# Kernel optimization log

Measured on AMD Instinct MI355X. Metric: run time of the kernel, lower is better.

Reference implementation:

```python
import jax, jax.numpy as jnp
import numpy as np

N_NODES = 50000
N_EDGES = 600000
N_FEAT = 128
HIDDEN = 128
OUT_CH = 128
N_GRAPHS = 64
BN_EPS = 1e-5


def gcn_conv(x, src, dst, ew, W, b):
    """PyG GCNConv: add self-loops, symmetric deg^{-1/2} normalization with edge weights."""
    n = x.shape[0]
    h = x @ W  # [N, out]
    loop = jnp.arange(n)
    src2 = jnp.concatenate([src, loop])
    dst2 = jnp.concatenate([dst, loop])
    w2 = jnp.concatenate([ew, jnp.ones((n,), x.dtype)])
    deg = jax.ops.segment_sum(w2, dst2, num_segments=n)
    dinv = jnp.where(deg > 0, jax.lax.rsqrt(deg), 0.0)
    norm = dinv[src2] * w2 * dinv[dst2]  # [E+N]
    out = jax.ops.segment_sum(h[src2] * norm[:, None], dst2, num_segments=n)
    return out + b


def setup_inputs() -> dict:
    key = jax.random.key(0)
    ks = jax.random.split(key, 12)
    x = jax.random.normal(ks[0], (N_NODES, N_FEAT), jnp.float32)
    edge_index = jax.random.randint(ks[1], (2, N_EDGES), 0, N_NODES, dtype=jnp.int64)
    batch = jnp.sort(jax.random.randint(ks[2], (N_NODES,), 0, N_GRAPHS, dtype=jnp.int64))
    edge_attr = jax.random.uniform(ks[3], (N_EDGES,), jnp.float32)
    s1 = 1.0 / np.sqrt(N_FEAT)
    s2 = 1.0 / np.sqrt(HIDDEN)
    s3 = 1.0 / np.sqrt(OUT_CH)
    s4 = 1.0 / np.sqrt(OUT_CH // 2)
    return {
        "x": x, "edge_index": edge_index, "batch": batch, "edge_attr": edge_attr,
        "W1": jax.random.uniform(ks[4], (N_FEAT, HIDDEN), jnp.float32, -s1, s1),
        "b1": jnp.zeros((HIDDEN,), jnp.float32),
        "W2": jax.random.uniform(ks[5], (HIDDEN, OUT_CH), jnp.float32, -s2, s2),
        "b2": jnp.zeros((OUT_CH,), jnp.float32),
        "fc1_W": jax.random.uniform(ks[6], (OUT_CH, OUT_CH // 2), jnp.float32, -s3, s3),
        "fc1_b": jax.random.uniform(ks[7], (OUT_CH // 2,), jnp.float32, -s3, s3),
        "bn_gamma": jnp.ones((OUT_CH // 2,), jnp.float32),
        "bn_beta": jnp.zeros((OUT_CH // 2,), jnp.float32),
        "fc3_W": jax.random.uniform(ks[8], (OUT_CH // 2, 1), jnp.float32, -s4, s4),
        "fc3_b": jax.random.uniform(ks[9], (1,), jnp.float32, -s4, s4),
    }


def reference(x, edge_index, batch, edge_attr, W1, b1, W2, b2,
              fc1_W, fc1_b, bn_gamma, bn_beta, fc3_W, fc3_b):
    src, dst = edge_index[0], edge_index[1]
    h = jax.nn.relu(gcn_conv(x, src, dst, edge_attr, W1, b1))
    # dropout skipped (deterministic eval: mode=False)
    h = jax.nn.relu(gcn_conv(h, src, dst, edge_attr, W2, b2))
    # global_mean_pool over batch segment ids
    sums = jax.ops.segment_sum(h, batch, num_segments=N_GRAPHS)  # [G, out]
    cnt = jax.ops.segment_sum(jnp.ones_like(batch, jnp.float32), batch, num_segments=N_GRAPHS)
    g = sums / jnp.maximum(cnt, 1.0)[:, None]
    z = jax.nn.relu(g @ fc1_W + fc1_b)
    # BatchNorm1d with batch statistics (training-mode math, biased var)
    mean = jnp.mean(z, axis=0)
    var = jnp.mean((z - mean) ** 2, axis=0)
    z = bn_gamma * (z - mean) * jax.lax.rsqrt(var + BN_EPS) + bn_beta
    return z @ fc3_W + fc3_b  # [G, 1]
```

## Files before the change

### kernel.cpp

```cpp
#include <hip/hip_runtime.h>

#define NNODES 50000
#define NEDGES 600000
#define NGRAPHS 64
#define BN_EPS 1e-5f
#define NB1 ((NNODES + 255) / 256)
#define PPG 16
#define GEMM_BLOCKS ((NNODES + 127) / 128)
#define NOWN 64
#define RANGE 782
#define SEG 16
#define SEGI4 (NEDGES / SEG / 4)
#define HIST_BLOCKS (NOWN * SEG)


__device__ __forceinline__ void gemm_tile(const float* __restrict__ A,
        const float* __restrict__ W, float* __restrict__ C, int block) {
    __shared__ float a_lds[32][132];
    __shared__ float w_lds[32][192];
    const int tid = threadIdx.x;
    const int row0 = block * 128;
    const int tx = tid & 15;
    const int ty = tid >> 4;
    float acc[4][8];
#pragma unroll
    for (int i = 0; i < 4; ++i)
#pragma unroll
        for (int j = 0; j < 8; ++j) acc[i][j] = 0.f;

    for (int kc = 0; kc < 128; kc += 32) {
#pragma unroll
        for (int p = 0; p < 2; ++p) {
            int idx = p * 512 + tid;
            int r = idx >> 3;
            int k4 = (idx & 7) << 2;
            int grow = row0 + r;
            float4 v = make_float4(0.f, 0.f, 0.f, 0.f);
            if (grow < NNODES) v = *(const float4*)(A + (size_t)grow * 128 + kc + k4);
            a_lds[k4 + 0][r] = v.x; a_lds[k4 + 1][r] = v.y;
            a_lds[k4 + 2][r] = v.z; a_lds[k4 + 3][r] = v.w;
        }
#pragma unroll
        for (int p = 0; p < 2; ++p) {
            int idx = p * 512 + tid;
            int kk = idx >> 5;
            int c4 = idx & 31;
            float4 v = *(const float4*)(W + (size_t)(kc + kk) * 128 + c4 * 4);
            int sw = 12 * (c4 >> 1) + ((c4 & 1) << 2);
            *(float4*)&w_lds[kk][sw] = v;
        }
        __syncthreads();
#pragma unroll
        for (int k = 0; k < 32; ++k) {
            float a[4], b[8];
            *(float4*)&a[0] = *(const float4*)&a_lds[k][ty * 4];
            *(float4*)&b[0] = *(const float4*)&w_lds[k][tx * 12];
            *(float4*)&b[4] = *(const float4*)&w_lds[k][tx * 12 + 4];
#pragma unroll
            for (int i = 0; i < 4; ++i)
#pragma unroll
                for (int j = 0; j < 8; ++j)
                    acc[i][j] = fmaf(a[i], b[j], acc[i][j]);
        }
        __syncthreads();
    }
#pragma unroll
    for (int i = 0; i < 4; ++i) {
        int grow = row0 + ty * 4 + i;
        if (grow < NNODES) {
            float4 v0 = make_float4(acc[i][0], acc[i][1], acc[i][2], acc[i][3]);
            float4 v1 = make_float4(acc[i][4], acc[i][5], acc[i][6], acc[i][7]);
            *(float4*)(C + (size_t)grow * 128 + tx * 8) = v0;
            *(float4*)(C + (size_t)grow * 128 + tx * 8 + 4) = v1;
        }
    }
}

__global__ __launch_bounds__(512) void k_gemm1_hist(const float* __restrict__ A,
        const float* __restrict__ W, float* __restrict__ C,
        const int* __restrict__ dst, int* __restrict__ cnt_seg) {
    if (blockIdx.x < HIST_BLOCKS) {
        __shared__ int lh[RANGE];
        int t = threadIdx.x;
        int own = blockIdx.x & (NOWN - 1);
        int seg = blockIdx.x >> 6;
        int lo = own * RANGE;
        int n = min(RANGE, NNODES - lo);
        for (int i = t; i < RANGE; i += 512) lh[i] = 0;
        __syncthreads();
        const int4* d4 = (const int4*)dst;
        int q1 = (seg + 1) * SEGI4;
        for (int q = seg * SEGI4 + t; q < q1; q += 512) {
            int4 v = d4[q];
            unsigned a0 = (unsigned)(v.x - lo);
            unsigned a1 = (unsigned)(v.y - lo);
            unsigned a2 = (unsigned)(v.z - lo);
            unsigned a3 = (unsigned)(v.w - lo);
            if (a0 < (unsigned)n) atomicAdd(&lh[a0], 1);
            if (a1 < (unsigned)n) atomicAdd(&lh[a1], 1);
            if (a2 < (unsigned)n) atomicAdd(&lh[a2], 1);
            if (a3 < (unsigned)n) atomicAdd(&lh[a3], 1);
        }
        __syncthreads();
        for (int i = t; i < n; i += 512) cnt_seg[(size_t)seg * NNODES + lo + i] = lh[i];
        return;
    }
    gemm_tile(A, W, C, blockIdx.x - HIST_BLOCKS);
}

__global__ __launch_bounds__(512) void k_gemm(const float* __restrict__ A,
        const float* __restrict__ W, float* __restrict__ C) {
    gemm_tile(A, W, C, blockIdx.x);
}


__global__ __launch_bounds__(256) void k_scan1(const int* __restrict__ cnt_seg,
        int* __restrict__ excl, int* __restrict__ bsum) {
    __shared__ int sh[256];
    int b = blockIdx.x, t = threadIdx.x;
    int idx = b * 256 + t;
    int v = 0;
    if (idx < NNODES) {
#pragma unroll
        for (int s = 0; s < SEG; ++s) v += cnt_seg[(size_t)s * NNODES + idx];
    }
    sh[t] = v;
    __syncthreads();
#pragma unroll
    for (int off = 1; off < 256; off <<= 1) {
        int x = (t >= off) ? sh[t - off] : 0;
        __syncthreads();
        sh[t] += x;
        __syncthreads();
    }
    if (idx < NNODES) excl[idx] = sh[t] - v;
    if (t == 255) bsum[b] = sh[255];
}

__global__ __launch_bounds__(256) void k_scan2(int* __restrict__ bsum) {
    __shared__ int sh[256];
    int t = threadIdx.x;
    int v = (t < NB1) ? bsum[t] : 0;
    sh[t] = v;
    __syncthreads();
#pragma unroll
    for (int off = 1; off < 256; off <<= 1) {
        int x = (t >= off) ? sh[t - off] : 0;
        __syncthreads();
        sh[t] += x;
        __syncthreads();
    }
    if (t < NB1) bsum[t] = sh[t] - v;
}

__global__ __launch_bounds__(256) void k_scan3(const int* __restrict__ excl,
        const int* __restrict__ bsum, int* __restrict__ row_start) {
    int b = blockIdx.x, t = threadIdx.x;
    int idx = b * 256 + t;
    if (idx < NNODES) row_start[idx] = excl[idx] + bsum[b];
    if (idx == 0) row_start[NNODES] = NEDGES;
}

__global__ __launch_bounds__(256) void k_base(const int* __restrict__ row_start,
        const int* __restrict__ cnt_seg, int* __restrict__ base) {
    int idx = blockIdx.x * 256 + threadIdx.x;
    if (idx >= NNODES) return;
    int run = row_start[idx];
#pragma unroll
    for (int s = 0; s < SEG; ++s) {
        int c = cnt_seg[(size_t)s * NNODES + idx];
        base[(size_t)s * NNODES + idx] = run;
        run += c;
    }
}


__global__ __launch_bounds__(512) void k_place_seg(const int* __restrict__ dst,
        const int* __restrict__ src, const float* __restrict__ ew,
        const int* __restrict__ base, int2* __restrict__ csr_pk) {
    __shared__ int lh[RANGE];
    int t = threadIdx.x;
    int own = blockIdx.x & (NOWN - 1);
    int seg = blockIdx.x >> 6;
    int lo = own * RANGE;
    int n = min(RANGE, NNODES - lo);
    for (int i = t; i < RANGE; i += 512) lh[i] = 0;
    __syncthreads();
    const int4* d4 = (const int4*)dst;
    int q1 = (seg + 1) * SEGI4;
    for (int q = seg * SEGI4 + t; q < q1; q += 512) {
        int4 v = d4[q];
        int e = q * 4;
        unsigned a0 = (unsigned)(v.x - lo);
        unsigned a1 = (unsigned)(v.y - lo);
        unsigned a2 = (unsigned)(v.z - lo);
        unsigned a3 = (unsigned)(v.w - lo);
        if (a0 < (unsigned)n) {
            int tk = atomicAdd(&lh[a0], 1);
            csr_pk[base[(size_t)seg * NNODES + v.x] + tk] =
                make_int2(src[e], __float_as_int(ew[e]));
        }
        if (a1 < (unsigned)n) {
            int tk = atomicAdd(&lh[a1], 1);
            csr_pk[base[(size_t)seg * NNODES + v.y] + tk] =
                make_int2(src[e + 1], __float_as_int(ew[e + 1]));
        }
        if (a2 < (unsigned)n) {
            int tk = atomicAdd(&lh[a2], 1);
            csr_pk[base[(size_t)seg * NNODES + v.z] + tk] =
                make_int2(src[e + 2], __float_as_int(ew[e + 2]));
        }
        if (a3 < (unsigned)n) {
            int tk = atomicAdd(&lh[a3], 1);
            csr_pk[base[(size_t)seg * NNODES + v.w] + tk] =
                make_int2(src[e + 3], __float_as_int(ew[e + 3]));
        }
    }
}

__global__ __launch_bounds__(256) void k_deg(const int* __restrict__ row_start,
        const int2* __restrict__ csr_pk, float* __restrict__ dinv) {
    int i = blockIdx.x * 256 + threadIdx.x;
    if (i >= NNODES) return;
    int e0 = row_start[i], e1 = row_start[i + 1];
    float deg = 1.f;
    for (int e = e0; e < e1; ++e) deg += __int_as_float(csr_pk[e].y);
    dinv[i] = rsqrtf(deg);
}

__global__ __launch_bounds__(256) void k_wfill(const int* __restrict__ row_start,
        int2* __restrict__ csr_pk, const float* __restrict__ dinv) {
    int i = blockIdx.x * 256 + threadIdx.x;
    if (i >= NNODES) return;
    int e0 = row_start[i], e1 = row_start[i + 1];
    float di = dinv[i];
    for (int e = e0; e < e1; ++e) {
        int2 pk = csr_pk[e];
        float w = dinv[pk.x] * __int_as_float(pk.y) * di;
        csr_pk[e].y = __float_as_int(w);
    }
}


__global__ __launch_bounds__(256) void k_aggregate(const float* __restrict__ h,
        const float* __restrict__ dinv, const int* __restrict__ row_start,
        const int2* __restrict__ csr_pk, const float* __restrict__ bias,
        float* __restrict__ out) {
    int gtid = blockIdx.x * 256 + threadIdx.x;
    int i = gtid >> 5;
    int lane = (gtid & 31) << 2;
    if (i >= NNODES) return;
    float di = dinv[i];
    float sw = di * di;
    float4 hv = *(const float4*)(h + (size_t)i * 128 + lane);
    float ax = sw * hv.x, ay = sw * hv.y, az = sw * hv.z, aw = sw * hv.w;
    int e = row_start[i];
    int e1 = row_start[i + 1];
    for (; e + 3 < e1; e += 4) {
        int2 p0 = csr_pk[e], p1 = csr_pk[e + 1], p2 = csr_pk[e + 2], p3 = csr_pk[e + 3];
        float4 v0 = *(const float4*)(h + (size_t)p0.x * 128 + lane);
        float4 v1 = *(const float4*)(h + (size_t)p1.x * 128 + lane);
        float4 v2 = *(const float4*)(h + (size_t)p2.x * 128 + lane);
        float4 v3 = *(const float4*)(h + (size_t)p3.x * 128 + lane);
        float w0 = __int_as_float(p0.y), w1 = __int_as_float(p1.y);
        float w2 = __int_as_float(p2.y), w3 = __int_as_float(p3.y);
        ax = fmaf(w0, v0.x, ax); ay = fmaf(w0, v0.y, ay);
        az = fmaf(w0, v0.z, az); aw = fmaf(w0, v0.w, aw);
        ax = fmaf(w1, v1.x, ax); ay = fmaf(w1, v1.y, ay);
        az = fmaf(w1, v1.z, az); aw = fmaf(w1, v1.w, aw);
        ax = fmaf(w2, v2.x, ax); ay = fmaf(w2, v2.y, ay);
        az = fmaf(w2, v2.z, az); aw = fmaf(w2, v2.w, aw);
        ax = fmaf(w3, v3.x, ax); ay = fmaf(w3, v3.y, ay);
        az = fmaf(w3, v3.z, az); aw = fmaf(w3, v3.w, aw);
    }
    for (; e < e1; ++e) {
        int2 p0 = csr_pk[e];
        float w0 = __int_as_float(p0.y);
        float4 v0 = *(const float4*)(h + (size_t)p0.x * 128 + lane);
        ax = fmaf(w0, v0.x, ax); ay = fmaf(w0, v0.y, ay);
        az = fmaf(w0, v0.z, az); aw = fmaf(w0, v0.w, aw);
    }
    float4 b = *(const float4*)(bias + lane);
    float4 o;
    o.x = fmaxf(ax + b.x, 0.f);
    o.y = fmaxf(ay + b.y, 0.f);
    o.z = fmaxf(az + b.z, 0.f);
    o.w = fmaxf(aw + b.w, 0.f);
    *(float4*)(out + (size_t)i * 128 + lane) = o;
}


__global__ __launch_bounds__(256) void k_pool1(const float* __restrict__ h2,
        const int* __restrict__ batch, float* __restrict__ part) {
    __shared__ float sh[256];
    int g = blockIdx.x / PPG;
    int p = blockIdx.x % PPG;
    int t = threadIdx.x;
    int lo = 0, hi = NNODES;
    while (lo < hi) { int mid = (lo + hi) >> 1; if (batch[mid] < g) lo = mid + 1; else hi = mid; }
    int b0 = lo;
    lo = 0; hi = NNODES;
    int g1 = g + 1;
    while (lo < hi) { int mid = (lo + hi) >> 1; if (batch[mid] < g1) lo = mid + 1; else hi = mid; }
    int b1 = lo;

    int c = t & 127, q = t >> 7;
    float acc = 0.f;
    for (int r = b0 + p * 2 + q; r < b1; r += PPG * 2) acc += h2[(size_t)r * 128 + c];
    sh[t] = acc;
    __syncthreads();
    if (t < 128) part[((size_t)g * PPG + p) * 128 + t] = sh[t] + sh[t + 128];
}

__global__ __launch_bounds__(128) void k_pool2(const float* __restrict__ part,
        const int* __restrict__ batch, float* __restrict__ gmean) {
    int g = blockIdx.x;
    int t = threadIdx.x;
    int lo = 0, hi = NNODES;
    while (lo < hi) { int mid = (lo + hi) >> 1; if (batch[mid] < g) lo = mid + 1; else hi = mid; }
    int b0 = lo;
    lo = 0; hi = NNODES;
    int g1 = g + 1;
    while (lo < hi) { int mid = (lo + hi) >> 1; if (batch[mid] < g1) lo = mid + 1; else hi = mid; }
    int b1 = lo;
    float s = 0.f;
#pragma unroll
    for (int p = 0; p < PPG; ++p) s += part[((size_t)g * PPG + p) * 128 + t];
    float n = (float)(b1 - b0);
    gmean[g * 128 + t] = s / fmaxf(n, 1.f);
}


__global__ __launch_bounds__(256) void k_head(const float* __restrict__ gmean,
        const float* __restrict__ fc1W, const float* __restrict__ fc1b,
        const float* __restrict__ gamma, const float* __restrict__ beta,
        const float* __restrict__ fc3W, const float* __restrict__ fc3b,
        float* __restrict__ out) {
    __shared__ float g[64][129];
    __shared__ float w[128][64];
    __shared__ float z[64][65];
    __shared__ float mu[64], isd[64];
    int t = threadIdx.x;
#pragma unroll
    for (int p = 0; p < 8; ++p) {
        int idx4 = p * 256 + t;
        int gg = idx4 >> 5;
        int c4 = (idx4 & 31) << 2;
        float4 v = *(const float4*)(gmean + gg * 128 + c4);
        *(float4*)&g[gg][c4] = v;
    }
#pragma unroll
    for (int p = 0; p < 8; ++p) {
        int idx4 = p * 256 + t;
        float4 v = *(const float4*)(fc1W + idx4 * 4);
        *(float4*)&w[0][idx4 * 4 - (idx4 >> 4) * 64 + (idx4 >> 4) * 64] = v;
    }
    __syncthreads();
    int r = t >> 2;
    int c0 = (t & 3) * 16;
    float acc[16];
#pragma unroll
    for (int j = 0; j < 16; ++j) acc[j] = 0.f;
    for (int k = 0; k < 128; ++k) {
        float gv = g[r][k];
#pragma unroll
        for (int j = 0; j < 16; ++j) acc[j] = fmaf(gv, w[k][c0 + j], acc[j]);
    }
#pragma unroll
    for (int j = 0; j < 16; ++j)
        z[r][c0 + j] = fmaxf(acc[j] + fc1b[c0 + j], 0.f);
    __syncthreads();
    if (t < 64) {
        float m = 0.f;
        for (int rr = 0; rr < 64; ++rr) m += z[rr][t];
        m *= (1.f / 64.f);
        float v = 0.f;
        for (int rr = 0; rr < 64; ++rr) { float d = z[rr][t] - m; v = fmaf(d, d, v); }
        v *= (1.f / 64.f);
        mu[t] = m;
        isd[t] = rsqrtf(v + BN_EPS);
    }
    __syncthreads();
    if (t < 64) {
        float a2 = fc3b[0];
        for (int cc = 0; cc < 64; ++cc) {
            float zn = fmaf(gamma[cc] * (z[t][cc] - mu[cc]), isd[cc], beta[cc]);
            a2 = fmaf(zn, fc3W[cc], a2);
        }
        out[t] = a2;
    }
}


extern "C" void kernel_launch(void* const* d_in, const int* in_sizes, int n_in,
                              void* d_out, int out_size, void* d_ws, size_t ws_size,
                              hipStream_t stream) {
    const float* x    = (const float*)d_in[0];
    const int*   ei   = (const int*)d_in[1];
    const int*   batch= (const int*)d_in[2];
    const float* ew   = (const float*)d_in[3];
    const float* W1   = (const float*)d_in[4];
    const float* b1   = (const float*)d_in[5];
    const float* W2   = (const float*)d_in[6];
    const float* b2   = (const float*)d_in[7];
    const float* fc1W = (const float*)d_in[8];
    const float* fc1b = (const float*)d_in[9];
    const float* gam  = (const float*)d_in[10];
    const float* bet  = (const float*)d_in[11];
    const float* fc3W = (const float*)d_in[12];
    const float* fc3b = (const float*)d_in[13];
    float* out = (float*)d_out;
    const int* srcp = ei;
    const int* dstp = ei + NEDGES;

    char* wsb = (char*)d_ws;
    size_t off = 0;
    auto alloc = [&](size_t bytes) {
        void* p = wsb + off;
        off = (off + bytes + 255) & ~(size_t)255;
        return p;
    };
    float* dinv      = (float*)alloc(NNODES * 4);
    int*   row_start = (int*)alloc((NNODES + 1) * 4);
    int*   cnt_seg   = (int*)alloc((size_t)SEG * NNODES * 4);
    int*   base      = (int*)alloc((size_t)SEG * NNODES * 4);
    int*   excl      = (int*)alloc(NNODES * 4);
    int*   bsum      = (int*)alloc(NB1 * 4);
    int2*  csr_pk    = (int2*)alloc((size_t)NEDGES * 8);
    float* hbuf      = (float*)alloc((size_t)NNODES * 128 * 4);
    float* abuf      = (float*)alloc((size_t)NNODES * 128 * 4);
    float* part      = (float*)alloc((size_t)NGRAPHS * PPG * 128 * 4);
    float* gmean     = (float*)alloc(NGRAPHS * 128 * 4);
    (void)ws_size; (void)in_sizes; (void)n_in; (void)out_size;

    k_gemm1_hist<<<HIST_BLOCKS + GEMM_BLOCKS, 512, 0, stream>>>(x, W1, hbuf, dstp, cnt_seg);
    k_scan1<<<NB1, 256, 0, stream>>>(cnt_seg, excl, bsum);
    k_scan2<<<1, 256, 0, stream>>>(bsum);
    k_scan3<<<NB1, 256, 0, stream>>>(excl, bsum, row_start);
    k_base<<<NB1, 256, 0, stream>>>(row_start, cnt_seg, base);
    k_place_seg<<<HIST_BLOCKS, 512, 0, stream>>>(dstp, srcp, ew, base, csr_pk);
    k_deg<<<NB1, 256, 0, stream>>>(row_start, csr_pk, dinv);
    k_wfill<<<NB1, 256, 0, stream>>>(row_start, csr_pk, dinv);

    k_aggregate<<<(NNODES * 32 + 255) / 256, 256, 0, stream>>>(hbuf, dinv, row_start,
                                                               csr_pk, b1, abuf);
    k_gemm<<<GEMM_BLOCKS, 512, 0, stream>>>(abuf, W2, hbuf);
    k_aggregate<<<(NNODES * 32 + 255) / 256, 256, 0, stream>>>(hbuf, dinv, row_start,
                                                               csr_pk, b2, abuf);
    k_pool1<<<NGRAPHS * PPG, 256, 0, stream>>>(abuf, batch, part);
    k_pool2<<<NGRAPHS, 128, 0, stream>>>(part, batch, gmean);
    k_head<<<1, 256, 0, stream>>>(gmean, fc1W, fc1b, gam, bet, fc3W, fc3b, out);
}
```

Baseline: 254.6 us.

## Shrink GEMM K-tile, reorder fused gemm/hist blocks, merge scan3 with base

Halves the GEMM K-chunk from 32 to 16, which halves LDS use per block and may allow more resident blocks, at the cost of twice as many barriers. Puts GEMM blocks ahead of histogram blocks in the fused first kernel so the heavier tiles dispatch first. Merges the scan3 and base kernels into one launch, removing a launch and a reread of row_start. Also simplifies an index expression in the head kernel.

```diff
diff --git a/kernel.cpp b/kernel.cpp
--- a/kernel.cpp
+++ b/kernel.cpp
@@ -16,8 +16,8 @@
 
 __device__ __forceinline__ void gemm_tile(const float* __restrict__ A,
         const float* __restrict__ W, float* __restrict__ C, int block) {
-    __shared__ float a_lds[32][132];
-    __shared__ float w_lds[32][192];
+    __shared__ float a_lds[16][132];
+    __shared__ float w_lds[16][192];
     const int tid = threadIdx.x;
     const int row0 = block * 128;
     const int tx = tid & 15;
@@ -28,30 +28,26 @@
 #pragma unroll
         for (int j = 0; j < 8; ++j) acc[i][j] = 0.f;
 
-    for (int kc = 0; kc < 128; kc += 32) {
-#pragma unroll
-        for (int p = 0; p < 2; ++p) {
-            int idx = p * 512 + tid;
-            int r = idx >> 3;
-            int k4 = (idx & 7) << 2;
+    for (int kc = 0; kc < 128; kc += 16) {
+        {
+            int r = tid >> 2;
+            int k4 = (tid & 3) << 2;
             int grow = row0 + r;
             float4 v = make_float4(0.f, 0.f, 0.f, 0.f);
             if (grow < NNODES) v = *(const float4*)(A + (size_t)grow * 128 + kc + k4);
             a_lds[k4 + 0][r] = v.x; a_lds[k4 + 1][r] = v.y;
             a_lds[k4 + 2][r] = v.z; a_lds[k4 + 3][r] = v.w;
         }
-#pragma unroll
-        for (int p = 0; p < 2; ++p) {
-            int idx = p * 512 + tid;
-            int kk = idx >> 5;
-            int c4 = idx & 31;
+        {
+            int kk = tid >> 5;
+            int c4 = tid & 31;
             float4 v = *(const float4*)(W + (size_t)(kc + kk) * 128 + c4 * 4);
             int sw = 12 * (c4 >> 1) + ((c4 & 1) << 2);
             *(float4*)&w_lds[kk][sw] = v;
         }
         __syncthreads();
 #pragma unroll
-        for (int k = 0; k < 32; ++k) {
+        for (int k = 0; k < 16; ++k) {
             float a[4], b[8];
             *(float4*)&a[0] = *(const float4*)&a_lds[k][ty * 4];
             *(float4*)&b[0] = *(const float4*)&w_lds[k][tx * 12];
@@ -79,11 +75,12 @@
 __global__ __launch_bounds__(512) void k_gemm1_hist(const float* __restrict__ A,
         const float* __restrict__ W, float* __restrict__ C,
         const int* __restrict__ dst, int* __restrict__ cnt_seg) {
-    if (blockIdx.x < HIST_BLOCKS) {
+    if (blockIdx.x >= GEMM_BLOCKS) {
         __shared__ int lh[RANGE];
         int t = threadIdx.x;
-        int own = blockIdx.x & (NOWN - 1);
-        int seg = blockIdx.x >> 6;
+        int hb = blockIdx.x - GEMM_BLOCKS;
+        int own = hb & (NOWN - 1);
+        int seg = hb >> 6;
         int lo = own * RANGE;
         int n = min(RANGE, NNODES - lo);
         for (int i = t; i < RANGE; i += 512) lh[i] = 0;
@@ -105,7 +102,7 @@
         for (int i = t; i < n; i += 512) cnt_seg[(size_t)seg * NNODES + lo + i] = lh[i];
         return;
     }
-    gemm_tile(A, W, C, blockIdx.x - HIST_BLOCKS);
+    gemm_tile(A, W, C, blockIdx.x);
 }
 
 __global__ __launch_bounds__(512) void k_gemm(const float* __restrict__ A,
@@ -153,19 +150,16 @@
     if (t < NB1) bsum[t] = sh[t] - v;
 }
 
-__global__ __launch_bounds__(256) void k_scan3(const int* __restrict__ excl,
-        const int* __restrict__ bsum, int* __restrict__ row_start) {
+__global__ __launch_bounds__(256) void k_scan3base(const int* __restrict__ excl,
+        const int* __restrict__ bsum, const int* __restrict__ cnt_seg,
+        int* __restrict__ row_start, int* __restrict__ base) {
     int b = blockIdx.x, t = threadIdx.x;
     int idx = b * 256 + t;
-    if (idx < NNODES) row_start[idx] = excl[idx] + bsum[b];
+    if (idx >= NNODES) return;
+    int rs = excl[idx] + bsum[b];
+    row_start[idx] = rs;
     if (idx == 0) row_start[NNODES] = NEDGES;
-}
-
-__global__ __launch_bounds__(256) void k_base(const int* __restrict__ row_start,
-        const int* __restrict__ cnt_seg, int* __restrict__ base) {
-    int idx = blockIdx.x * 256 + threadIdx.x;
-    if (idx >= NNODES) return;
-    int run = row_start[idx];
+    int run = rs;
 #pragma unroll
     for (int s = 0; s < SEG; ++s) {
         int c = cnt_seg[(size_t)s * NNODES + idx];
@@ -353,7 +347,7 @@
     for (int p = 0; p < 8; ++p) {
         int idx4 = p * 256 + t;
         float4 v = *(const float4*)(fc1W + idx4 * 4);
-        *(float4*)&w[0][idx4 * 4 - (idx4 >> 4) * 64 + (idx4 >> 4) * 64] = v;
+        ((float4*)&w[0][0])[idx4] = v;
     }
     __syncthreads();
     int r = t >> 2;
@@ -433,11 +427,10 @@
     float* gmean     = (float*)alloc(NGRAPHS * 128 * 4);
     (void)ws_size; (void)in_sizes; (void)n_in; (void)out_size;
 
-    k_gemm1_hist<<<HIST_BLOCKS + GEMM_BLOCKS, 512, 0, stream>>>(x, W1, hbuf, dstp, cnt_seg);
+    k_gemm1_hist<<<GEMM_BLOCKS + HIST_BLOCKS, 512, 0, stream>>>(x, W1, hbuf, dstp, cnt_seg);
     k_scan1<<<NB1, 256, 0, stream>>>(cnt_seg, excl, bsum);
     k_scan2<<<1, 256, 0, stream>>>(bsum);
-    k_scan3<<<NB1, 256, 0, stream>>>(excl, bsum, row_start);
-    k_base<<<NB1, 256, 0, stream>>>(row_start, cnt_seg, base);
+    k_scan3base<<<NB1, 256, 0, stream>>>(excl, bsum, cnt_seg, row_start, base);
     k_place_seg<<<HIST_BLOCKS, 512, 0, stream>>>(dstp, srcp, ew, base, csr_pk);
     k_deg<<<NB1, 256, 0, stream>>>(row_start, csr_pk, dinv);
     k_wfill<<<NB1, 256, 0, stream>>>(row_start, csr_pk, dinv);
```

Measured after the change: 242.1 us. 4.9% less time.
